# Performance work log

Hardware: AMD Instinct MI355X
Metric: run time of the kernel (lower is better)

## Reference

```python
import jax, jax.numpy as jnp
import numpy as np

R = 4            # num_runs
P_DROP = 0.2     # node dropout prob
BN_EPS = 1e-5
L = 2            # num_layers
D = 128          # hidden_channels
NA, NP_ = 50000, 100000
E = 500000


def setup_inputs() -> dict:
    key = jax.random.key(0)
    ks = jax.random.split(key, 20)
    s = 0.05
    x_author = jax.random.normal(ks[0], (NA, D), jnp.float32)
    x_paper = jax.random.normal(ks[1], (NP_, D), jnp.float32)
    # edge_index rows: [src, dst]
    ei_ap = jnp.stack([
        jax.random.randint(ks[2], (E,), 0, NA),
        jax.random.randint(ks[3], (E,), 0, NP_)]).astype(jnp.int64)
    ei_pa = jnp.stack([
        jax.random.randint(ks[4], (E,), 0, NP_),
        jax.random.randint(ks[5], (E,), 0, NA)]).astype(jnp.int64)
    # bernoulli(1-p) keep masks, one per run per node
    drop_author = (jax.random.uniform(ks[6], (R, NA)) < (1.0 - P_DROP)).astype(jnp.float32)
    drop_paper = (jax.random.uniform(ks[7], (R, NP_)) < (1.0 - P_DROP)).astype(jnp.float32)
    return {
        "x_author": x_author, "x_paper": x_paper,
        "ei_ap": ei_ap, "ei_pa": ei_pa,
        "drop_author": drop_author, "drop_paper": drop_paper,
        "lin_a_w": jax.random.normal(ks[8], (D, D)) * s,
        "lin_a_b": jnp.zeros((D,), jnp.float32),
        "lin_p_w": jax.random.normal(ks[9], (D, D)) * s,
        "lin_p_b": jnp.zeros((D,), jnp.float32),
        "W1": jax.random.normal(ks[10], (L, 2, D, D)) * s,
        "B1": jnp.zeros((L, 2, D), jnp.float32),
        "G": jnp.ones((L, 2, D), jnp.float32),
        "BT": jnp.zeros((L, 2, D), jnp.float32),
        "W2": jax.random.normal(ks[11], (L, 2, D, D)) * s,
        "B2": jnp.zeros((L, 2, D), jnp.float32),
        "EPS": jnp.zeros((L, 2), jnp.float32),  # GIN train_eps init 0
        "final_w": jax.random.normal(ks[12], (D, 4)) * s,
        "final_b": jnp.zeros((4,), jnp.float32),
    }


def _gin(x_src, x_dst, ei, eps, w1, b1, g, bt, w2, b2):
    # x_src: [Rs*Ns, D] flattened over runs; x_dst: [Rd*Nd, D]
    # scatter-sum neighbor messages into dst (only run-0 slots touched,
    # matching the original code which reuses the unexpanded edge_index)
    agg = jnp.zeros_like(x_dst).at[ei[1]].add(x_src[ei[0]])
    z = (1.0 + eps) * x_dst + agg
    h = z @ w1 + b1
    # BatchNorm1d, training-mode batch stats (biased variance)
    mu = h.mean(axis=0)
    var = ((h - mu) ** 2).mean(axis=0)
    h = (h - mu) * jax.lax.rsqrt(var + BN_EPS) * g + bt
    h = jax.nn.relu(h)
    return h @ w2 + b2


def reference(x_author, x_paper, ei_ap, ei_pa, drop_author, drop_paper,
              lin_a_w, lin_a_b, lin_p_w, lin_p_b,
              W1, B1, G, BT, W2, B2, EPS, final_w, final_b):
    inv_keep = 1.0 / (1.0 - P_DROP)
    # input projections, expand over runs, DropGNN node dropout
    h_a = x_author @ lin_a_w + lin_a_b                       # [Na, D]
    h_a = jnp.broadcast_to(h_a[None], (R,) + h_a.shape)      # [R, Na, D]
    h_a = h_a * drop_author[..., None] * inv_keep
    h_p = x_paper @ lin_p_w + lin_p_b
    h_p = jnp.broadcast_to(h_p[None], (R,) + h_p.shape)
    h_p = h_p * drop_paper[..., None] * inv_keep

    for l in range(L):
        xa = h_a.reshape(-1, D)
        xp = h_p.reshape(-1, D)
        # edge type 0: author -writes-> paper ; edge type 1: paper -> author
        new_p = _gin(xa, xp, ei_ap, EPS[l, 0], W1[l, 0], B1[l, 0], G[l, 0], BT[l, 0], W2[l, 0], B2[l, 0])
        new_a = _gin(xp, xa, ei_pa, EPS[l, 1], W1[l, 1], B1[l, 1], G[l, 1], BT[l, 1], W2[l, 1], B2[l, 1])
        h_a = jax.nn.relu(new_a.reshape(R, NA, D))
        h_p = jax.nn.relu(new_p.reshape(R, NP_, D))

    h = h_a.mean(axis=0)                                     # [Na, D]
    return h @ final_w + final_b                             # [Na, num_classes]
```

## Files before the change

kernel.cpp:

```cpp
#include <hip/hip_runtime.h>

#define NRUNS 4
#define NAU 50000
#define NPP 100000
#define NEDGE 500000
#define HD 128
#define INV_KEEP 1.25f
#define BN_EPS 1e-5f
#define LDA 136
#define NB_GEMM 1536

#define M_PROJ 0
#define M_GIN1 1
#define M_GIN2 2

typedef unsigned short bf16r;
typedef __attribute__((ext_vector_type(8))) short v8s;
typedef __attribute__((ext_vector_type(4))) float v4f;

__device__ inline float bf2f(bf16r u) {
    return __uint_as_float(((unsigned)u) << 16);
}
__device__ inline bf16r f2bf(float f) {
    __bf16 b = (__bf16)f;
    return __builtin_bit_cast(bf16r, b);
}

__global__ __launch_bounds__(256)
void zero_k(float* p, long n4) {
    long i = (long)blockIdx.x * 256 + threadIdx.x;
    long stride = (long)gridDim.x * 256;
    float4 z = make_float4(0.f, 0.f, 0.f, 0.f);
    for (; i < n4; i += stride) ((float4*)p)[i] = z;
}

__global__ __launch_bounds__(256)
void convw_k(const float* __restrict__ lin_a_w, const float* __restrict__ lin_p_w,
             const float* __restrict__ W1, const float* __restrict__ W2,
             bf16r* __restrict__ wt)
{
    int t = blockIdx.x >> 6;
    int e = (blockIdx.x & 63) * 256 + threadIdx.x;
    const float* src;
    if (t == 0) src = lin_a_w;
    else if (t == 1) src = lin_p_w;
    else if (t < 6) src = W1 + (size_t)(t - 2) * HD * HD;
    else src = W2 + (size_t)(t - 6) * HD * HD;
    int n = e >> 7, k = e & 127;
    wt[(size_t)t * HD * HD + e] = f2bf(src[(size_t)k * HD + n]);
}

__global__ __launch_bounds__(256)
void count_k(const int* __restrict__ ei, int E, int* cnt) {
    int e = blockIdx.x * 256 + threadIdx.x;
    if (e < E) atomicAdd(&cnt[ei[E + e]], 1);
}

__global__ __launch_bounds__(256)
void scan1_k(const int* __restrict__ in, int* out, int* partial, int n) {
    __shared__ int lds[256];
    int b = blockIdx.x, t = threadIdx.x;
    int base = b * 1024 + t * 4;
    int v0 = 0, v1 = 0, v2 = 0, v3 = 0;
    if (base + 3 < n) {
        int4 x = *(const int4*)(in + base);
        v0 = x.x; v1 = x.y; v2 = x.z; v3 = x.w;
    } else {
        if (base + 0 < n) v0 = in[base + 0];
        if (base + 1 < n) v1 = in[base + 1];
        if (base + 2 < n) v2 = in[base + 2];
        if (base + 3 < n) v3 = in[base + 3];
    }
    int s = v0 + v1 + v2 + v3;
    lds[t] = s;
    __syncthreads();
    for (int d = 1; d < 256; d <<= 1) {
        int x = (t >= d) ? lds[t - d] : 0;
        __syncthreads();
        lds[t] += x;
        __syncthreads();
    }
    int excl = lds[t] - s;
    if (base + 0 < n) out[base + 0] = excl;
    if (base + 1 < n) out[base + 1] = excl + v0;
    if (base + 2 < n) out[base + 2] = excl + v0 + v1;
    if (base + 3 < n) out[base + 3] = excl + v0 + v1 + v2;
    if (t == 255) partial[b] = lds[255];
}

__global__ __launch_bounds__(256)
void scan2_k(int* partial, int n) {
    __shared__ int lds[256];
    int t = threadIdx.x;
    int s = (t < n) ? partial[t] : 0;
    lds[t] = s;
    __syncthreads();
    for (int d = 1; d < 256; d <<= 1) {
        int x = (t >= d) ? lds[t - d] : 0;
        __syncthreads();
        lds[t] += x;
        __syncthreads();
    }
    if (t < n) partial[t] = lds[t] - s;
}

__global__ __launch_bounds__(256)
void scan3_k(int* off, int* cur, const int* __restrict__ partial, int n, int total) {
    int b = blockIdx.x, t = threadIdx.x;
    int add = partial[b];
    int base = b * 1024 + t * 4;
    #pragma unroll
    for (int j = 0; j < 4; ++j) {
        int i = base + j;
        if (i < n) {
            int v = off[i] + add;
            off[i] = v;
            cur[i] = v;
        }
    }
    if (b == 0 && t == 0) off[n] = total;
}

__global__ __launch_bounds__(256)
void fill_k(const int* __restrict__ ei, int E, int* cur, int* bucket) {
    int e = blockIdx.x * 256 + threadIdx.x;
    if (e < E) {
        int d = ei[E + e];
        int p = atomicAdd(&cur[d], 1);
        bucket[p] = ei[e];
    }
}

__global__ __launch_bounds__(256)
void gather2_k(const bf16r* __restrict__ hA, const bf16r* __restrict__ hP,
               bf16r* __restrict__ aggP, bf16r* __restrict__ aggA,
               const int* __restrict__ offAP, const int* __restrict__ bktAP,
               const int* __restrict__ offPA, const int* __restrict__ bktPA)
{
    int gw = (blockIdx.x * 256 + threadIdx.x) >> 6;
    int lane = threadIdx.x & 63;
    const bf16r* src; bf16r* agg; const int* off; const int* bkt; int w;
    if (gw < NPP) { src = hA; agg = aggP; off = offAP; bkt = bktAP; w = gw; }
    else          { src = hP; agg = aggA; off = offPA; bkt = bktPA; w = gw - NPP; }
    int s0 = off[w], s1 = off[w + 1];
    float a0 = 0.f, a1 = 0.f;
    int e = s0;
    for (; e + 1 < s1; e += 2) {
        int i0 = bkt[e], i1 = bkt[e + 1];
        ushort2 u = *(const ushort2*)(src + (size_t)i0 * HD + lane * 2);
        ushort2 v = *(const ushort2*)(src + (size_t)i1 * HD + lane * 2);
        a0 += bf2f(u.x) + bf2f(v.x);
        a1 += bf2f(u.y) + bf2f(v.y);
    }
    if (e < s1) {
        ushort2 u = *(const ushort2*)(src + (size_t)bkt[e] * HD + lane * 2);
        a0 += bf2f(u.x);
        a1 += bf2f(u.y);
    }
    ushort2 o;
    o.x = f2bf(a0);
    o.y = f2bf(a1);
    *(ushort2*)(agg + (size_t)w * HD + lane * 2) = o;
}

__global__ __launch_bounds__(256)
void scatter_k(const bf16r* __restrict__ src, float* dst,
               const int* __restrict__ ei, int E)
{
    int g = blockIdx.x * 256 + threadIdx.x;
    int e = g >> 5, lane = g & 31;
    if (e >= E) return;
    int s = ei[e], d = ei[E + e];
    ushort4 u = *(const ushort4*)(src + (size_t)s * HD + lane * 4);
    float* dp = dst + (size_t)d * HD + lane * 4;
    unsafeAtomicAdd(dp + 0, bf2f(u.x));
    unsafeAtomicAdd(dp + 1, bf2f(u.y));
    unsafeAtomicAdd(dp + 2, bf2f(u.z));
    unsafeAtomicAdd(dp + 3, bf2f(u.w));
}

struct SideP {
    const void* in;
    bf16r* out;
    const bf16r* wt;
    const float* bias;
    const void* agg;
    const float* epsp;
    float* gsum;
    float* gsumsq;
    const float* scale;
    const float* shift;
    const float* mask;
    int M, Nn, tiles;
};

template<int MODE, typename IT, typename AT>
__global__ __launch_bounds__(256)
void mfma_gemm(SideP P, SideP A, int BP)
{
    __shared__ bf16r za[64][LDA];
    __shared__ float red[2][HD];
    const int tid = threadIdx.x;

    SideP S;
    int t, tstride;
    if ((int)blockIdx.x < BP) { S = P; t = blockIdx.x; tstride = BP; }
    else { S = A; t = (int)blockIdx.x - BP; tstride = NB_GEMM - BP; }
    if (t >= S.tiles) return;

    const int wid = tid >> 6, lane = tid & 63;
    const int lr = lane & 15, lk = (lane >> 4) * 8;
    const int colq = (lane >> 4) * 4, cb = wid * 32;
    const int srow = tid >> 4;
    const int scol = (tid & 15) * 8;

    float epsv = 1.0f;
    if (MODE == M_GIN1) epsv = 1.0f + S.epsp[0];

    v8s w[2][4];
    #pragma unroll
    for (int cf = 0; cf < 2; ++cf)
        #pragma unroll
        for (int ks = 0; ks < 4; ++ks)
            w[cf][ks] = *(const v8s*)(S.wt + (size_t)(cb + cf * 16 + lr) * HD + ks * 32 + lk);

    const float4 bb0 = *(const float4*)(S.bias + cb + colq);
    const float4 bb1 = *(const float4*)(S.bias + cb + 16 + colq);

    float4 sc0h, sc1h, sh0h, sh1h;
    if (MODE == M_GIN2) {
        sc0h = *(const float4*)(S.scale + scol);
        sc1h = *(const float4*)(S.scale + scol + 4);
        sh0h = *(const float4*)(S.shift + scol);
        sh1h = *(const float4*)(S.shift + scol + 4);
    }

    float st_s[2][4], st_q[2][4];
    if (MODE == M_GIN1) {
        #pragma unroll
        for (int cf = 0; cf < 2; ++cf)
            #pragma unroll
            for (int j = 0; j < 4; ++j) { st_s[cf][j] = 0.f; st_q[cf][j] = 0.f; }
    }

    constexpr int NVH = (MODE == M_PROJ) ? 2 : 1;
    constexpr bool PAGG = (MODE == M_GIN1);
    constexpr int NVA = (PAGG && sizeof(AT) == 4) ? 2 : 1;
    int4 pre[4][NVH];
    int4 preA[4][NVA];

    auto prefetch = [&](int tt) {
        int m0n = tt * 64;
        #pragma unroll
        for (int i = 0; i < 4; ++i) {
            int gr = m0n + srow + 16 * i;
            if (gr < S.M) {
                const int4* p = (const int4*)((const IT*)S.in + (size_t)gr * HD + scol);
                pre[i][0] = p[0];
                if constexpr (NVH == 2) pre[i][1] = p[1];
            } else {
                pre[i][0] = make_int4(0, 0, 0, 0);
                if constexpr (NVH == 2) pre[i][1] = make_int4(0, 0, 0, 0);
            }
            if constexpr (PAGG) {
                if (gr < S.Nn) {
                    const int4* pa = (const int4*)((const AT*)S.agg + (size_t)gr * HD + scol);
                    preA[i][0] = pa[0];
                    if constexpr (NVA == 2) preA[i][1] = pa[1];
                } else {
                    preA[i][0] = make_int4(0, 0, 0, 0);
                    if constexpr (NVA == 2) preA[i][1] = make_int4(0, 0, 0, 0);
                }
            }
        }
    };

    prefetch(t);

    for (;;) {
        const int m0 = t * 64;
        #pragma unroll
        for (int i = 0; i < 4; ++i) {
            int row = srow + 16 * i;
            float v[8];
            if constexpr (NVH == 2) {
                const float* pf = (const float*)&pre[i][0];
                #pragma unroll
                for (int j = 0; j < 8; ++j) v[j] = pf[j];
            } else {
                const bf16r* pu = (const bf16r*)&pre[i][0];
                #pragma unroll
                for (int j = 0; j < 8; ++j) v[j] = bf2f(pu[j]);
            }
            if constexpr (MODE == M_GIN1) {
                float av[8];
                if constexpr (sizeof(AT) == 4) {
                    const float* pa = (const float*)&preA[i][0];
                    #pragma unroll
                    for (int j = 0; j < 8; ++j) av[j] = pa[j];
                } else {
                    const bf16r* pa = (const bf16r*)&preA[i][0];
                    #pragma unroll
                    for (int j = 0; j < 8; ++j) av[j] = bf2f(pa[j]);
                }
                #pragma unroll
                for (int j = 0; j < 8; ++j) v[j] = v[j] * epsv + av[j];
            } else if constexpr (MODE == M_GIN2) {
                v[0] = fmaxf(v[0] * sc0h.x + sh0h.x, 0.f);
                v[1] = fmaxf(v[1] * sc0h.y + sh0h.y, 0.f);
                v[2] = fmaxf(v[2] * sc0h.z + sh0h.z, 0.f);
                v[3] = fmaxf(v[3] * sc0h.w + sh0h.w, 0.f);
                v[4] = fmaxf(v[4] * sc1h.x + sh1h.x, 0.f);
                v[5] = fmaxf(v[5] * sc1h.y + sh1h.y, 0.f);
                v[6] = fmaxf(v[6] * sc1h.z + sh1h.z, 0.f);
                v[7] = fmaxf(v[7] * sc1h.w + sh1h.w, 0.f);
            }
            union { v8s w8; bf16r u[8]; } pk;
            #pragma unroll
            for (int j = 0; j < 8; ++j) pk.u[j] = f2bf(v[j]);
            *(v8s*)&za[row][scol] = pk.w8;
        }
        __syncthreads();

        const int tn = t + tstride;
        const bool more = tn < S.tiles;
        if (more) prefetch(tn);

        v4f acc[2][4];
        #pragma unroll
        for (int cf = 0; cf < 2; ++cf)
            #pragma unroll
            for (int rf = 0; rf < 4; ++rf) acc[cf][rf] = (v4f){0.f, 0.f, 0.f, 0.f};

        #pragma unroll
        for (int ks = 0; ks < 4; ++ks)
            #pragma unroll
            for (int rf = 0; rf < 4; ++rf) {
                v8s a = *(const v8s*)&za[rf * 16 + lr][ks * 32 + lk];
                acc[0][rf] = __builtin_amdgcn_mfma_f32_16x16x32_bf16(w[0][ks], a, acc[0][rf], 0, 0, 0);
                acc[1][rf] = __builtin_amdgcn_mfma_f32_16x16x32_bf16(w[1][ks], a, acc[1][rf], 0, 0, 0);
            }

        #pragma unroll
        for (int rf = 0; rf < 4; ++rf) {
            acc[0][rf][0] += bb0.x; acc[0][rf][1] += bb0.y;
            acc[0][rf][2] += bb0.z; acc[0][rf][3] += bb0.w;
            acc[1][rf][0] += bb1.x; acc[1][rf][1] += bb1.y;
            acc[1][rf][2] += bb1.z; acc[1][rf][3] += bb1.w;
        }

        if constexpr (MODE == M_PROJ) {
            #pragma unroll
            for (int rf = 0; rf < 4; ++rf) {
                int grow = m0 + rf * 16 + lr;
                if (grow < S.M) {
                    #pragma unroll
                    for (int run = 0; run < NRUNS; ++run) {
                        float wm = S.mask[(size_t)run * S.Nn + grow] * INV_KEEP;
                        #pragma unroll
                        for (int cf = 0; cf < 2; ++cf) {
                            ushort4 o;
                            o.x = f2bf(acc[cf][rf][0] * wm);
                            o.y = f2bf(acc[cf][rf][1] * wm);
                            o.z = f2bf(acc[cf][rf][2] * wm);
                            o.w = f2bf(acc[cf][rf][3] * wm);
                            *(ushort4*)(S.out + ((size_t)run * S.Nn + grow) * HD + cb + cf * 16 + colq) = o;
                        }
                    }
                }
            }
        } else if constexpr (MODE == M_GIN1) {
            #pragma unroll
            for (int rf = 0; rf < 4; ++rf) {
                int grow = m0 + rf * 16 + lr;
                #pragma unroll
                for (int cf = 0; cf < 2; ++cf) {
                    ushort4 o;
                    o.x = f2bf(acc[cf][rf][0]);
                    o.y = f2bf(acc[cf][rf][1]);
                    o.z = f2bf(acc[cf][rf][2]);
                    o.w = f2bf(acc[cf][rf][3]);
                    *(ushort4*)(S.out + (size_t)grow * HD + cb + cf * 16 + colq) = o;
                }
            }
            #pragma unroll
            for (int cf = 0; cf < 2; ++cf)
                #pragma unroll
                for (int j = 0; j < 4; ++j)
                    #pragma unroll
                    for (int rf = 0; rf < 4; ++rf) {
                        float vv = acc[cf][rf][j];
                        st_s[cf][j] += vv;
                        st_q[cf][j] += vv * vv;
                    }
        } else {
            #pragma unroll
            for (int rf = 0; rf < 4; ++rf) {
                int grow = m0 + rf * 16 + lr;
                #pragma unroll
                for (int cf = 0; cf < 2; ++cf) {
                    ushort4 o;
                    o.x = f2bf(fmaxf(acc[cf][rf][0], 0.f));
                    o.y = f2bf(fmaxf(acc[cf][rf][1], 0.f));
                    o.z = f2bf(fmaxf(acc[cf][rf][2], 0.f));
                    o.w = f2bf(fmaxf(acc[cf][rf][3], 0.f));
                    *(ushort4*)(S.out + (size_t)grow * HD + cb + cf * 16 + colq) = o;
                }
            }
        }

        if (!more) break;
        t = tn;
        __syncthreads();
    }

    if constexpr (MODE == M_GIN1) {
        #pragma unroll
        for (int d = 1; d < 16; d <<= 1)
            #pragma unroll
            for (int cf = 0; cf < 2; ++cf)
                #pragma unroll
                for (int j = 0; j < 4; ++j) {
                    st_s[cf][j] += __shfl_xor(st_s[cf][j], d);
                    st_q[cf][j] += __shfl_xor(st_q[cf][j], d);
                }
        if (lr == 0) {
            #pragma unroll
            for (int cf = 0; cf < 2; ++cf)
                #pragma unroll
                for (int j = 0; j < 4; ++j) {
                    red[0][cb + cf * 16 + colq + j] = st_s[cf][j];
                    red[1][cb + cf * 16 + colq + j] = st_q[cf][j];
                }
        }
        __syncthreads();
        if (tid < HD) {
            unsafeAtomicAdd(S.gsum + tid, red[0][tid]);
            unsafeAtomicAdd(S.gsumsq + tid, red[1][tid]);
        }
    }
}

__global__ void finalize2_k(float* gsP, float* gsqP, const float* gamP, const float* betP,
                            float* scP, float* shP, float invNP,
                            float* gsA, float* gsqA, const float* gamA, const float* betA,
                            float* scA, float* shA, float invNA)
{
    int c = threadIdx.x;
    float *gs, *gsq, *sc, *sh;
    const float *gm, *bt;
    float invN;
    if (c < HD) { gs = gsP; gsq = gsqP; gm = gamP; bt = betP; sc = scP; sh = shP; invN = invNP; }
    else { c -= HD; gs = gsA; gsq = gsqA; gm = gamA; bt = betA; sc = scA; sh = shA; invN = invNA; }
    float mu = gs[c] * invN;
    float var = gsq[c] * invN - mu * mu;
    float s = gm[c] * rsqrtf(var + BN_EPS);
    sc[c] = s;
    sh[c] = bt[c] - mu * s;
    gs[c] = 0.f;
    gsq[c] = 0.f;
}

__global__ __launch_bounds__(256)
void final_k(const bf16r* __restrict__ ha, const float* __restrict__ fw,
             const float* __restrict__ fb, float* __restrict__ out)
{
    int g = blockIdx.x * 256 + threadIdx.x;
    int node = g >> 6, lane = g & 63;
    if (node >= NAU) return;
    float m0 = 0.f, m1 = 0.f;
    #pragma unroll
    for (int r = 0; r < NRUNS; ++r) {
        size_t base = ((size_t)r * NAU + node) * HD;
        m0 += bf2f(ha[base + lane]);
        m1 += bf2f(ha[base + 64 + lane]);
    }
    m0 *= 0.25f;
    m1 *= 0.25f;
    float p[4];
    #pragma unroll
    for (int c = 0; c < 4; ++c)
        p[c] = m0 * fw[lane * 4 + c] + m1 * fw[(lane + 64) * 4 + c];
    #pragma unroll
    for (int off = 32; off >= 1; off >>= 1)
        #pragma unroll
        for (int c = 0; c < 4; ++c) p[c] += __shfl_down(p[c], off);
    if (lane == 0) {
        #pragma unroll
        for (int c = 0; c < 4; ++c) out[(size_t)node * 4 + c] = p[c] + fb[c];
    }
}

#define CSR_INTS ((size_t)(NPP + 4) + NEDGE + (NAU + 4) + NEDGE)
#define WT_ELEMS ((size_t)10 * HD * HD)

template<bool GATHER>
static void run_all(void* const* d_in, void* d_out, void* d_ws, hipStream_t stream)
{
    const float* x_author = (const float*)d_in[0];
    const float* x_paper  = (const float*)d_in[1];
    const int*   ei_ap    = (const int*)d_in[2];
    const int*   ei_pa    = (const int*)d_in[3];
    const float* drop_a   = (const float*)d_in[4];
    const float* drop_p   = (const float*)d_in[5];
    const float* lin_a_w  = (const float*)d_in[6];
    const float* lin_a_b  = (const float*)d_in[7];
    const float* lin_p_w  = (const float*)d_in[8];
    const float* lin_p_b  = (const float*)d_in[9];
    const float* W1       = (const float*)d_in[10];
    const float* B1       = (const float*)d_in[11];
    const float* G        = (const float*)d_in[12];
    const float* BT       = (const float*)d_in[13];
    const float* W2       = (const float*)d_in[14];
    const float* B2       = (const float*)d_in[15];
    const float* EPS      = (const float*)d_in[16];
    const float* fw       = (const float*)d_in[17];
    const float* fb       = (const float*)d_in[18];

    float* gsumP   = (float*)d_ws;
    float* gsumsqP = gsumP + HD;
    float* gsumA   = gsumP + 2 * HD;
    float* gsumsqA = gsumP + 3 * HD;
    float* scP     = gsumP + 4 * HD;
    float* shP     = gsumP + 5 * HD;
    float* scA     = gsumP + 6 * HD;
    float* shA     = gsumP + 7 * HD;
    bf16r* wt = (bf16r*)(gsumP + 8 * HD);
    char* cp = (char*)(wt + WT_ELEMS);

    int *off_ap = nullptr, *bkt_ap = nullptr, *off_pa = nullptr, *bkt_pa = nullptr;
    if (GATHER) {
        int* ip = (int*)cp;
        off_ap = ip;  ip += NPP + 4;
        bkt_ap = ip;  ip += NEDGE;
        off_pa = ip;  ip += NAU + 4;
        bkt_pa = ip;  ip += NEDGE;
        cp = (char*)ip;
    }
    void* agg_a_v = cp;
    size_t aggElem = GATHER ? sizeof(bf16r) : sizeof(float);
    void* agg_p_v = cp + (size_t)NAU * HD * aggElem;
    bf16r* h_a = (bf16r*)(cp + (size_t)(NAU + NPP) * HD * aggElem);
    bf16r* h_p = h_a + (size_t)NRUNS * NAU * HD;

    const bf16r* wt_lin_a = wt;
    const bf16r* wt_lin_p = wt + (size_t)1 * HD * HD;
    const bf16r* wt_W1    = wt + (size_t)2 * HD * HD;
    const bf16r* wt_W2    = wt + (size_t)6 * HD * HD;

    convw_k<<<640, 256, 0, stream>>>(lin_a_w, lin_p_w, W1, W2, wt);
    zero_k<<<1, 256, 0, stream>>>(gsumP, (4 * HD) / 4);

    if (GATHER) {
        int* cur_ap  = (int*)agg_a_v;
        int* cur_pa  = cur_ap + NPP;
        int* partial = cur_pa + NAU;
        {
            int nchunk = (NPP + 1023) / 1024;
            zero_k<<<64, 256, 0, stream>>>((float*)cur_ap, NPP / 4);
            count_k<<<(NEDGE + 255) / 256, 256, 0, stream>>>(ei_ap, NEDGE, cur_ap);
            scan1_k<<<nchunk, 256, 0, stream>>>(cur_ap, off_ap, partial, NPP);
            scan2_k<<<1, 256, 0, stream>>>(partial, nchunk);
            scan3_k<<<nchunk, 256, 0, stream>>>(off_ap, cur_ap, partial, NPP, NEDGE);
            fill_k<<<(NEDGE + 255) / 256, 256, 0, stream>>>(ei_ap, NEDGE, cur_ap, bkt_ap);
        }
        {
            int nchunk = (NAU + 1023) / 1024;
            zero_k<<<64, 256, 0, stream>>>((float*)cur_pa, NAU / 4);
            count_k<<<(NEDGE + 255) / 256, 256, 0, stream>>>(ei_pa, NEDGE, cur_pa);
            scan1_k<<<nchunk, 256, 0, stream>>>(cur_pa, off_pa, partial, NAU);
            scan2_k<<<1, 256, 0, stream>>>(partial, nchunk);
            scan3_k<<<nchunk, 256, 0, stream>>>(off_pa, cur_pa, partial, NAU, NEDGE);
            fill_k<<<(NEDGE + 255) / 256, 256, 0, stream>>>(ei_pa, NEDGE, cur_pa, bkt_pa);
        }
    }

    SideP Pp = {};
    Pp.in = x_paper; Pp.out = h_p; Pp.wt = wt_lin_p; Pp.bias = lin_p_b;
    Pp.mask = drop_p; Pp.M = NPP; Pp.Nn = NPP; Pp.tiles = (NPP + 63) / 64;
    SideP Pa = {};
    Pa.in = x_author; Pa.out = h_a; Pa.wt = wt_lin_a; Pa.bias = lin_a_b;
    Pa.mask = drop_a; Pa.M = NAU; Pa.Nn = NAU; Pa.tiles = (NAU + 63) / 64;
    int BPproj = (int)((long)NB_GEMM * Pp.tiles / (Pp.tiles + Pa.tiles));
    mfma_gemm<M_PROJ, float, bf16r><<<NB_GEMM, 256, 0, stream>>>(Pp, Pa, BPproj);

    const int TP = NRUNS * NPP / 64, TA = NRUNS * NAU / 64;
    const int BPgin = (int)((long)NB_GEMM * TP / (TP + TA));

    for (int l = 0; l < 2; ++l) {
        int t0 = l * 2 + 0, t1 = l * 2 + 1;

        if (GATHER) {
            gather2_k<<<((NPP + NAU) * 64) / 256, 256, 0, stream>>>(
                h_a, h_p, (bf16r*)agg_p_v, (bf16r*)agg_a_v,
                off_ap, bkt_ap, off_pa, bkt_pa);
        } else {
            zero_k<<<2048, 256, 0, stream>>>((float*)agg_a_v, ((size_t)(NAU + NPP) * HD) / 4);
            scatter_k<<<(NEDGE * 32) / 256, 256, 0, stream>>>(h_a, (float*)agg_p_v, ei_ap, NEDGE);
            scatter_k<<<(NEDGE * 32) / 256, 256, 0, stream>>>(h_p, (float*)agg_a_v, ei_pa, NEDGE);
        }

        SideP G1p = {};
        G1p.in = h_p; G1p.out = h_p; G1p.wt = wt_W1 + (size_t)t0 * HD * HD;
        G1p.bias = B1 + (size_t)t0 * HD; G1p.agg = agg_p_v; G1p.epsp = EPS + t0;
        G1p.gsum = gsumP; G1p.gsumsq = gsumsqP;
        G1p.M = NRUNS * NPP; G1p.Nn = NPP; G1p.tiles = TP;
        SideP G1a = {};
        G1a.in = h_a; G1a.out = h_a; G1a.wt = wt_W1 + (size_t)t1 * HD * HD;
        G1a.bias = B1 + (size_t)t1 * HD; G1a.agg = agg_a_v; G1a.epsp = EPS + t1;
        G1a.gsum = gsumA; G1a.gsumsq = gsumsqA;
        G1a.M = NRUNS * NAU; G1a.Nn = NAU; G1a.tiles = TA;
        if (GATHER)
            mfma_gemm<M_GIN1, bf16r, bf16r><<<NB_GEMM, 256, 0, stream>>>(G1p, G1a, BPgin);
        else
            mfma_gemm<M_GIN1, bf16r, float><<<NB_GEMM, 256, 0, stream>>>(G1p, G1a, BPgin);

        finalize2_k<<<1, 256, 0, stream>>>(
            gsumP, gsumsqP, G + (size_t)t0 * HD, BT + (size_t)t0 * HD, scP, shP,
            1.0f / (NRUNS * NPP),
            gsumA, gsumsqA, G + (size_t)t1 * HD, BT + (size_t)t1 * HD, scA, shA,
            1.0f / (NRUNS * NAU));

        SideP G2p = {};
        G2p.in = h_p; G2p.out = h_p; G2p.wt = wt_W2 + (size_t)t0 * HD * HD;
        G2p.bias = B2 + (size_t)t0 * HD; G2p.scale = scP; G2p.shift = shP;
        G2p.M = NRUNS * NPP; G2p.Nn = NPP; G2p.tiles = TP;
        SideP G2a = {};
        G2a.in = h_a; G2a.out = h_a; G2a.wt = wt_W2 + (size_t)t1 * HD * HD;
        G2a.bias = B2 + (size_t)t1 * HD; G2a.scale = scA; G2a.shift = shA;
        G2a.M = NRUNS * NAU; G2a.Nn = NAU; G2a.tiles = TA;
        mfma_gemm<M_GIN2, bf16r, bf16r><<<NB_GEMM, 256, 0, stream>>>(G2p, G2a, BPgin);
    }

    final_k<<<(NAU * 64) / 256, 256, 0, stream>>>(h_a, fw, fb, (float*)d_out);
}

extern "C" void kernel_launch(void* const* d_in, const int* in_sizes, int n_in,
                              void* d_out, int out_size, void* d_ws, size_t ws_size,
                              hipStream_t stream)
{
    const size_t hB    = (size_t)NRUNS * (NAU + NPP) * HD * sizeof(bf16r);
    const size_t statB = 8 * HD * sizeof(float);
    const size_t wtB   = WT_ELEMS * sizeof(bf16r);
    const size_t csrB  = CSR_INTS * sizeof(int);
    const size_t aggBF = (size_t)(NAU + NPP) * HD * sizeof(bf16r);

    const size_t need_gather = statB + wtB + csrB + aggBF + hB;
    if (ws_size >= need_gather) {
        run_all<true>(d_in, d_out, d_ws, stream);
    } else {
        run_all<false>(d_in, d_out, d_ws, stream);
    }
}
```

Measured before the change: 650.0 us.

## Fuse CSR gather and dropout into GIN1 GEMM, merge CSR-build and finalize kernels

The projection GEMM now writes a single unexpanded bf16 copy. The first GIN GEMM applies dropout masks on the fly and gathers neighbour rows through the CSR directly, so the separate gather kernel and the aggregate buffer are gone. BatchNorm scale and shift are computed inside the second GEMM, replacing the finalize kernel. The CSR-build, weight-conversion and zeroing kernels are merged across both edge types, and the GEMM grid size is lowered. The cost is more irregular gathers inside the GEMM's load phase, which may stall the MFMA pipeline and unbalance work across blocks.

```diff
diff --git a/kernel.cpp b/kernel.cpp
--- a/kernel.cpp
+++ b/kernel.cpp
@@ -8,11 +8,17 @@
 #define INV_KEEP 1.25f
 #define BN_EPS 1e-5f
 #define LDA 136
-#define NB_GEMM 1536
-
-#define M_PROJ 0
-#define M_GIN1 1
-#define M_GIN2 2
+#define NB_GEMM 1280
+
+#define M_PROJ   0
+#define M_GIN1   1
+#define M_GIN2   2
+#define M_PROJ1  3
+#define M_GIN1F0 4
+#define M_GIN1F1 5
+
+#define C_AP ((NPP + 1023) / 1024)
+#define C_PA ((NAU + 1023) / 1024)
 
 typedef unsigned short bf16r;
 typedef __attribute__((ext_vector_type(8))) short v8s;
@@ -35,32 +41,49 @@
 }
 
 __global__ __launch_bounds__(256)
-void convw_k(const float* __restrict__ lin_a_w, const float* __restrict__ lin_p_w,
-             const float* __restrict__ W1, const float* __restrict__ W2,
-             bf16r* __restrict__ wt)
-{
-    int t = blockIdx.x >> 6;
-    int e = (blockIdx.x & 63) * 256 + threadIdx.x;
-    const float* src;
-    if (t == 0) src = lin_a_w;
-    else if (t == 1) src = lin_p_w;
-    else if (t < 6) src = W1 + (size_t)(t - 2) * HD * HD;
-    else src = W2 + (size_t)(t - 6) * HD * HD;
-    int n = e >> 7, k = e & 127;
-    wt[(size_t)t * HD * HD + e] = f2bf(src[(size_t)k * HD + n]);
-}
-
-__global__ __launch_bounds__(256)
-void count_k(const int* __restrict__ ei, int E, int* cnt) {
-    int e = blockIdx.x * 256 + threadIdx.x;
-    if (e < E) atomicAdd(&cnt[ei[E + e]], 1);
-}
-
-__global__ __launch_bounds__(256)
-void scan1_k(const int* __restrict__ in, int* out, int* partial, int n) {
+void convw_prep_k(const float* __restrict__ lin_a_w, const float* __restrict__ lin_p_w,
+                  const float* __restrict__ W1, const float* __restrict__ W2,
+                  bf16r* __restrict__ wt, float* __restrict__ stats,
+                  float* __restrict__ curz, int curz4)
+{
+    int b = blockIdx.x;
+    if (b < 640) {
+        int t = b >> 6;
+        int e = (b & 63) * 256 + threadIdx.x;
+        const float* src;
+        if (t == 0) src = lin_a_w;
+        else if (t == 1) src = lin_p_w;
+        else if (t < 6) src = W1 + (size_t)(t - 2) * HD * HD;
+        else src = W2 + (size_t)(t - 6) * HD * HD;
+        int n = e >> 7, k = e & 127;
+        wt[(size_t)t * HD * HD + e] = f2bf(src[(size_t)k * HD + n]);
+    } else if (b == 640) {
+        ((float4*)stats)[threadIdx.x] = make_float4(0.f, 0.f, 0.f, 0.f);
+    } else {
+        int i = (b - 641) * 256 + threadIdx.x;
+        if (i < curz4) ((float4*)curz)[i] = make_float4(0.f, 0.f, 0.f, 0.f);
+    }
+}
+
+__global__ __launch_bounds__(256)
+void count2_k(const int* __restrict__ ei_ap, const int* __restrict__ ei_pa,
+              int* curA, int* curB)
+{
+    int g = blockIdx.x * 256 + threadIdx.x;
+    if (g < NEDGE) atomicAdd(&curA[ei_ap[NEDGE + g]], 1);
+    else if (g < 2 * NEDGE) atomicAdd(&curB[ei_pa[NEDGE + (g - NEDGE)]], 1);
+}
+
+__global__ __launch_bounds__(256)
+void scan1m_k(const int* __restrict__ curA, int* offA,
+              const int* __restrict__ curB, int* offB, int* partial)
+{
     __shared__ int lds[256];
     int b = blockIdx.x, t = threadIdx.x;
-    int base = b * 1024 + t * 4;
+    const int* in; int* out; int n, chunk;
+    if (b < C_AP) { in = curA; out = offA; n = NPP; chunk = b; }
+    else          { in = curB; out = offB; n = NAU; chunk = b - C_AP; }
+    int base = chunk * 1024 + t * 4;
     int v0 = 0, v1 = 0, v2 = 0, v3 = 0;
     if (base + 3 < n) {
         int4 x = *(const int4*)(in + base);
@@ -89,10 +112,13 @@
 }
 
 __global__ __launch_bounds__(256)
-void scan2_k(int* partial, int n) {
+void scan2m_k(int* partial)
+{
     __shared__ int lds[256];
     int t = threadIdx.x;
-    int s = (t < n) ? partial[t] : 0;
+    int base = blockIdx.x == 0 ? 0 : C_AP;
+    int n = blockIdx.x == 0 ? C_AP : C_PA;
+    int s = (t < n) ? partial[base + t] : 0;
     lds[t] = s;
     __syncthreads();
     for (int d = 1; d < 256; d <<= 1) {
@@ -101,14 +127,19 @@
         lds[t] += x;
         __syncthreads();
     }
-    if (t < n) partial[t] = lds[t] - s;
-}
-
-__global__ __launch_bounds__(256)
-void scan3_k(int* off, int* cur, const int* __restrict__ partial, int n, int total) {
+    if (t < n) partial[base + t] = lds[t] - s;
+}
+
+__global__ __launch_bounds__(256)
+void scan3m_k(int* offA, int* curA, int* offB, int* curB,
+              const int* __restrict__ partial)
+{
     int b = blockIdx.x, t = threadIdx.x;
+    int* off; int* cur; int n, chunk;
+    if (b < C_AP) { off = offA; cur = curA; n = NPP; chunk = b; }
+    else          { off = offB; cur = curB; n = NAU; chunk = b - C_AP; }
     int add = partial[b];
-    int base = b * 1024 + t * 4;
+    int base = chunk * 1024 + t * 4;
     #pragma unroll
     for (int j = 0; j < 4; ++j) {
         int i = base + j;
@@ -118,49 +149,22 @@
             cur[i] = v;
         }
     }
-    if (b == 0 && t == 0) off[n] = total;
-}
-
-__global__ __launch_bounds__(256)
-void fill_k(const int* __restrict__ ei, int E, int* cur, int* bucket) {
-    int e = blockIdx.x * 256 + threadIdx.x;
-    if (e < E) {
-        int d = ei[E + e];
-        int p = atomicAdd(&cur[d], 1);
-        bucket[p] = ei[e];
-    }
-}
-
-__global__ __launch_bounds__(256)
-void gather2_k(const bf16r* __restrict__ hA, const bf16r* __restrict__ hP,
-               bf16r* __restrict__ aggP, bf16r* __restrict__ aggA,
-               const int* __restrict__ offAP, const int* __restrict__ bktAP,
-               const int* __restrict__ offPA, const int* __restrict__ bktPA)
-{
-    int gw = (blockIdx.x * 256 + threadIdx.x) >> 6;
-    int lane = threadIdx.x & 63;
-    const bf16r* src; bf16r* agg; const int* off; const int* bkt; int w;
-    if (gw < NPP) { src = hA; agg = aggP; off = offAP; bkt = bktAP; w = gw; }
-    else          { src = hP; agg = aggA; off = offPA; bkt = bktPA; w = gw - NPP; }
-    int s0 = off[w], s1 = off[w + 1];
-    float a0 = 0.f, a1 = 0.f;
-    int e = s0;
-    for (; e + 1 < s1; e += 2) {
-        int i0 = bkt[e], i1 = bkt[e + 1];
-        ushort2 u = *(const ushort2*)(src + (size_t)i0 * HD + lane * 2);
-        ushort2 v = *(const ushort2*)(src + (size_t)i1 * HD + lane * 2);
-        a0 += bf2f(u.x) + bf2f(v.x);
-        a1 += bf2f(u.y) + bf2f(v.y);
-    }
-    if (e < s1) {
-        ushort2 u = *(const ushort2*)(src + (size_t)bkt[e] * HD + lane * 2);
-        a0 += bf2f(u.x);
-        a1 += bf2f(u.y);
-    }
-    ushort2 o;
-    o.x = f2bf(a0);
-    o.y = f2bf(a1);
-    *(ushort2*)(agg + (size_t)w * HD + lane * 2) = o;
+    if (chunk == 0 && t == 0) off[n] = NEDGE;
+}
+
+__global__ __launch_bounds__(256)
+void fill2_k(const int* __restrict__ ei_ap, const int* __restrict__ ei_pa,
+             int* curA, int* bktA, int* curB, int* bktB)
+{
+    int g = blockIdx.x * 256 + threadIdx.x;
+    if (g < NEDGE) {
+        int d = ei_ap[NEDGE + g];
+        bktA[atomicAdd(&curA[d], 1)] = ei_ap[g];
+    } else if (g < 2 * NEDGE) {
+        int e = g - NEDGE;
+        int d = ei_pa[NEDGE + e];
+        bktB[atomicAdd(&curB[d], 1)] = ei_pa[e];
+    }
 }
 
 __global__ __launch_bounds__(256)
@@ -181,15 +185,22 @@
 
 struct SideP {
     const void* in;
+    const void* in2;
     bf16r* out;
+    bf16r* out2;
+    const bf16r* src;
+    const int* off;
+    const int* bkt;
+    const float* msk0;
     const bf16r* wt;
     const float* bias;
     const void* agg;
     const float* epsp;
     float* gsum;
     float* gsumsq;
-    const float* scale;
-    const float* shift;
+    const float* gamma;
+    const float* beta;
+    float invN;
     const float* mask;
     int M, Nn, tiles;
 };
@@ -208,6 +219,12 @@
     else { S = A; t = (int)blockIdx.x - BP; tstride = NB_GEMM - BP; }
     if (t >= S.tiles) return;
 
+    constexpr bool FUSED   = (MODE == M_GIN1F0 || MODE == M_GIN1F1);
+    constexpr bool MASKF   = (MODE == M_GIN1F0);
+    constexpr bool GIN1ANY = (MODE == M_GIN1 || FUSED);
+    constexpr int  NVH     = (MODE == M_PROJ || MODE == M_PROJ1) ? 2 : 1;
+    constexpr bool PAGG    = (MODE == M_GIN1);
+
     const int wid = tid >> 6, lane = tid & 63;
     const int lr = lane & 15, lk = (lane >> 4) * 8;
     const int colq = (lane >> 4) * 4, cb = wid * 32;
@@ -215,7 +232,7 @@
     const int scol = (tid & 15) * 8;
 
     float epsv = 1.0f;
-    if (MODE == M_GIN1) epsv = 1.0f + S.epsp[0];
+    if (GIN1ANY) epsv = 1.0f + S.epsp[0];
 
     v8s w[2][4];
     #pragma unroll
@@ -227,34 +244,53 @@
     const float4 bb0 = *(const float4*)(S.bias + cb + colq);
     const float4 bb1 = *(const float4*)(S.bias + cb + 16 + colq);
 
-    float4 sc0h, sc1h, sh0h, sh1h;
-    if (MODE == M_GIN2) {
-        sc0h = *(const float4*)(S.scale + scol);
-        sc1h = *(const float4*)(S.scale + scol + 4);
-        sh0h = *(const float4*)(S.shift + scol);
-        sh1h = *(const float4*)(S.shift + scol + 4);
+    float sc8[MODE == M_GIN2 ? 8 : 1], sh8[MODE == M_GIN2 ? 8 : 1];
+    if constexpr (MODE == M_GIN2) {
+        #pragma unroll
+        for (int j = 0; j < 8; ++j) {
+            int c = scol + j;
+            float mu = S.gsum[c] * S.invN;
+            float var = S.gsumsq[c] * S.invN - mu * mu;
+            float s = S.gamma[c] * rsqrtf(var + BN_EPS);
+            sc8[j] = s;
+            sh8[j] = S.beta[c] - mu * s;
+        }
     }
 
     float st_s[2][4], st_q[2][4];
-    if (MODE == M_GIN1) {
+    if (GIN1ANY) {
         #pragma unroll
         for (int cf = 0; cf < 2; ++cf)
             #pragma unroll
             for (int j = 0; j < 4; ++j) { st_s[cf][j] = 0.f; st_q[cf][j] = 0.f; }
     }
 
-    constexpr int NVH = (MODE == M_PROJ) ? 2 : 1;
-    constexpr bool PAGG = (MODE == M_GIN1);
     constexpr int NVA = (PAGG && sizeof(AT) == 4) ? 2 : 1;
     int4 pre[4][NVH];
     int4 preA[4][NVA];
+    float mpre[MASKF ? 4 : 1];
+    int2 offv[FUSED ? 4 : 1];
 
     auto prefetch = [&](int tt) {
         int m0n = tt * 64;
         #pragma unroll
         for (int i = 0; i < 4; ++i) {
             int gr = m0n + srow + 16 * i;
-            if (gr < S.M) {
+            if constexpr (FUSED) {
+                int run = (gr >= S.Nn) + (gr >= 2 * S.Nn) + (gr >= 3 * S.Nn);
+                size_t sidx = MASKF ? (size_t)(gr - run * S.Nn) : (size_t)gr;
+                pre[i][0] = *(const int4*)((const bf16r*)S.in + sidx * HD + scol);
+                if constexpr (MASKF) mpre[i] = S.mask[gr];
+                if (gr < S.Nn) {
+                    offv[i].x = S.off[gr];
+                    offv[i].y = S.off[gr + 1];
+                } else {
+                    offv[i] = make_int2(0, 0);
+                }
+            } else if constexpr (MODE == M_GIN2) {
+                const IT* base = (const IT*)((gr < S.Nn) ? S.in2 : S.in);
+                pre[i][0] = *(const int4*)(base + (size_t)gr * HD + scol);
+            } else if (gr < S.M) {
                 const int4* p = (const int4*)((const IT*)S.in + (size_t)gr * HD + scol);
                 pre[i][0] = p[0];
                 if constexpr (NVH == 2) pre[i][1] = p[1];
@@ -292,7 +328,28 @@
                 #pragma unroll
                 for (int j = 0; j < 8; ++j) v[j] = bf2f(pu[j]);
             }
-            if constexpr (MODE == M_GIN1) {
+            if constexpr (FUSED) {
+                float coef = epsv;
+                if constexpr (MASKF) coef *= mpre[i] * INV_KEEP;
+                float g[8];
+                #pragma unroll
+                for (int j = 0; j < 8; ++j) g[j] = 0.f;
+                int s0 = offv[i].x, s1 = offv[i].y;
+                for (int e = s0; e < s1; ++e) {
+                    int idx = S.bkt[e];
+                    float m = 1.0f;
+                    if constexpr (MASKF) m = S.msk0[idx] * INV_KEEP;
+                    const bf16r* rp = S.src + (size_t)idx * HD + scol;
+                    ushort4 u0 = *(const ushort4*)rp;
+                    ushort4 u1 = *(const ushort4*)(rp + 4);
+                    g[0] += m * bf2f(u0.x); g[1] += m * bf2f(u0.y);
+                    g[2] += m * bf2f(u0.z); g[3] += m * bf2f(u0.w);
+                    g[4] += m * bf2f(u1.x); g[5] += m * bf2f(u1.y);
+                    g[6] += m * bf2f(u1.z); g[7] += m * bf2f(u1.w);
+                }
+                #pragma unroll
+                for (int j = 0; j < 8; ++j) v[j] = v[j] * coef + g[j];
+            } else if constexpr (MODE == M_GIN1) {
                 float av[8];
                 if constexpr (sizeof(AT) == 4) {
                     const float* pa = (const float*)&preA[i][0];
@@ -306,14 +363,9 @@
                 #pragma unroll
                 for (int j = 0; j < 8; ++j) v[j] = v[j] * epsv + av[j];
             } else if constexpr (MODE == M_GIN2) {
-                v[0] = fmaxf(v[0] * sc0h.x + sh0h.x, 0.f);
-                v[1] = fmaxf(v[1] * sc0h.y + sh0h.y, 0.f);
-                v[2] = fmaxf(v[2] * sc0h.z + sh0h.z, 0.f);
-                v[3] = fmaxf(v[3] * sc0h.w + sh0h.w, 0.f);
-                v[4] = fmaxf(v[4] * sc1h.x + sh1h.x, 0.f);
-                v[5] = fmaxf(v[5] * sc1h.y + sh1h.y, 0.f);
-                v[6] = fmaxf(v[6] * sc1h.z + sh1h.z, 0.f);
-                v[7] = fmaxf(v[7] * sc1h.w + sh1h.w, 0.f);
+                #pragma unroll
+                for (int j = 0; j < 8; ++j)
+                    v[j] = fmaxf(v[j] * sc8[j] + sh8[j], 0.f);
             }
             union { v8s w8; bf16r u[8]; } pk;
             #pragma unroll
@@ -369,10 +421,30 @@
                     }
                 }
             }
-        } else if constexpr (MODE == M_GIN1) {
+        } else if constexpr (MODE == M_PROJ1) {
             #pragma unroll
             for (int rf = 0; rf < 4; ++rf) {
                 int grow = m0 + rf * 16 + lr;
+                if (grow < S.M) {
+                    #pragma unroll
+                    for (int cf = 0; cf < 2; ++cf) {
+                        ushort4 o;
+                        o.x = f2bf(acc[cf][rf][0]);
+                        o.y = f2bf(acc[cf][rf][1]);
+                        o.z = f2bf(acc[cf][rf][2]);
+                        o.w = f2bf(acc[cf][rf][3]);
+                        *(ushort4*)(S.out + (size_t)grow * HD + cb + cf * 16 + colq) = o;
+                    }
+                }
+            }
+        } else if constexpr (GIN1ANY) {
+            #pragma unroll
+            for (int rf = 0; rf < 4; ++rf) {
+                int grow = m0 + rf * 16 + lr;
+                bf16r* ob = S.out;
+                if constexpr (MODE == M_GIN1F1) {
+                    if (grow < S.Nn) ob = S.out2;
+                }
                 #pragma unroll
                 for (int cf = 0; cf < 2; ++cf) {
                     ushort4 o;
@@ -380,7 +452,7 @@
                     o.y = f2bf(acc[cf][rf][1]);
                     o.z = f2bf(acc[cf][rf][2]);
                     o.w = f2bf(acc[cf][rf][3]);
-                    *(ushort4*)(S.out + (size_t)grow * HD + cb + cf * 16 + colq) = o;
+                    *(ushort4*)(ob + (size_t)grow * HD + cb + cf * 16 + colq) = o;
                 }
             }
             #pragma unroll
@@ -414,7 +486,7 @@
         __syncthreads();
     }
 
-    if constexpr (MODE == M_GIN1) {
+    if constexpr (GIN1ANY) {
         #pragma unroll
         for (int d = 1; d < 16; d <<= 1)
             #pragma unroll
@@ -439,26 +511,6 @@
             unsafeAtomicAdd(S.gsumsq + tid, red[1][tid]);
         }
     }
-}
-
-__global__ void finalize2_k(float* gsP, float* gsqP, const float* gamP, const float* betP,
-                            float* scP, float* shP, float invNP,
-                            float* gsA, float* gsqA, const float* gamA, const float* betA,
-                            float* scA, float* shA, float invNA)
-{
-    int c = threadIdx.x;
-    float *gs, *gsq, *sc, *sh;
-    const float *gm, *bt;
-    float invN;
-    if (c < HD) { gs = gsP; gsq = gsqP; gm = gamP; bt = betP; sc = scP; sh = shP; invN = invNP; }
-    else { c -= HD; gs = gsA; gsq = gsqA; gm = gamA; bt = betA; sc = scA; sh = shA; invN = invNA; }
-    float mu = gs[c] * invN;
-    float var = gsq[c] * invN - mu * mu;
-    float s = gm[c] * rsqrtf(var + BN_EPS);
-    sc[c] = s;
-    sh[c] = bt[c] - mu * s;
-    gs[c] = 0.f;
-    gsq[c] = 0.f;
 }
 
 __global__ __launch_bounds__(256)
@@ -517,15 +569,8 @@
     const float* fw       = (const float*)d_in[17];
     const float* fb       = (const float*)d_in[18];
 
-    float* gsumP   = (float*)d_ws;
-    float* gsumsqP = gsumP + HD;
-    float* gsumA   = gsumP + 2 * HD;
-    float* gsumsqA = gsumP + 3 * HD;
-    float* scP     = gsumP + 4 * HD;
-    float* shP     = gsumP + 5 * HD;
-    float* scA     = gsumP + 6 * HD;
-    float* shA     = gsumP + 7 * HD;
-    bf16r* wt = (bf16r*)(gsumP + 8 * HD);
+    float* stats = (float*)d_ws;
+    bf16r* wt = (bf16r*)(stats + 8 * HD);
     char* cp = (char*)(wt + WT_ELEMS);
 
     int *off_ap = nullptr, *bkt_ap = nullptr, *off_pa = nullptr, *bkt_pa = nullptr;
@@ -537,10 +582,18 @@
         bkt_pa = ip;  ip += NEDGE;
         cp = (char*)ip;
     }
-    void* agg_a_v = cp;
-    size_t aggElem = GATHER ? sizeof(bf16r) : sizeof(float);
-    void* agg_p_v = cp + (size_t)NAU * HD * aggElem;
-    bf16r* h_a = (bf16r*)(cp + (size_t)(NAU + NPP) * HD * aggElem);
+
+    bf16r* alt_a = nullptr; bf16r* alt_p = nullptr;
+    void* agg_a_v = nullptr; void* agg_p_v = nullptr;
+    if (GATHER) {
+        alt_a = (bf16r*)cp;  cp += (size_t)NAU * HD * sizeof(bf16r);
+        alt_p = (bf16r*)cp;  cp += (size_t)NPP * HD * sizeof(bf16r);
+    } else {
+        agg_a_v = cp;
+        agg_p_v = cp + (size_t)NAU * HD * sizeof(float);
+        cp += (size_t)(NAU + NPP) * HD * sizeof(float);
+    }
+    bf16r* h_a = (bf16r*)cp;
     bf16r* h_p = h_a + (size_t)NRUNS * NAU * HD;
 
     const bf16r* wt_lin_a = wt;
@@ -548,88 +601,116 @@
     const bf16r* wt_W1    = wt + (size_t)2 * HD * HD;
     const bf16r* wt_W2    = wt + (size_t)6 * HD * HD;
 
-    convw_k<<<640, 256, 0, stream>>>(lin_a_w, lin_p_w, W1, W2, wt);
-    zero_k<<<1, 256, 0, stream>>>(gsumP, (4 * HD) / 4);
+    int* cur_ap = GATHER ? (int*)alt_a : (int*)agg_a_v;
+    int* cur_pa = cur_ap + NPP;
+    int* partial = cur_pa + NAU;
+
+    convw_prep_k<<<788, 256, 0, stream>>>(lin_a_w, lin_p_w, W1, W2, wt, stats,
+                                          (float*)cur_ap, (NPP + NAU) / 4);
 
     if (GATHER) {
-        int* cur_ap  = (int*)agg_a_v;
-        int* cur_pa  = cur_ap + NPP;
-        int* partial = cur_pa + NAU;
-        {
-            int nchunk = (NPP + 1023) / 1024;
-            zero_k<<<64, 256, 0, stream>>>((float*)cur_ap, NPP / 4);
-            count_k<<<(NEDGE + 255) / 256, 256, 0, stream>>>(ei_ap, NEDGE, cur_ap);
-            scan1_k<<<nchunk, 256, 0, stream>>>(cur_ap, off_ap, partial, NPP);
-            scan2_k<<<1, 256, 0, stream>>>(partial, nchunk);
-            scan3_k<<<nchunk, 256, 0, stream>>>(off_ap, cur_ap, partial, NPP, NEDGE);
-            fill_k<<<(NEDGE + 255) / 256, 256, 0, stream>>>(ei_ap, NEDGE, cur_ap, bkt_ap);
-        }
-        {
-            int nchunk = (NAU + 1023) / 1024;
-            zero_k<<<64, 256, 0, stream>>>((float*)cur_pa, NAU / 4);
-            count_k<<<(NEDGE + 255) / 256, 256, 0, stream>>>(ei_pa, NEDGE, cur_pa);
-            scan1_k<<<nchunk, 256, 0, stream>>>(cur_pa, off_pa, partial, NAU);
-            scan2_k<<<1, 256, 0, stream>>>(partial, nchunk);
-            scan3_k<<<nchunk, 256, 0, stream>>>(off_pa, cur_pa, partial, NAU, NEDGE);
-            fill_k<<<(NEDGE + 255) / 256, 256, 0, stream>>>(ei_pa, NEDGE, cur_pa, bkt_pa);
-        }
-    }
-
-    SideP Pp = {};
-    Pp.in = x_paper; Pp.out = h_p; Pp.wt = wt_lin_p; Pp.bias = lin_p_b;
-    Pp.mask = drop_p; Pp.M = NPP; Pp.Nn = NPP; Pp.tiles = (NPP + 63) / 64;
-    SideP Pa = {};
-    Pa.in = x_author; Pa.out = h_a; Pa.wt = wt_lin_a; Pa.bias = lin_a_b;
-    Pa.mask = drop_a; Pa.M = NAU; Pa.Nn = NAU; Pa.tiles = (NAU + 63) / 64;
-    int BPproj = (int)((long)NB_GEMM * Pp.tiles / (Pp.tiles + Pa.tiles));
-    mfma_gemm<M_PROJ, float, bf16r><<<NB_GEMM, 256, 0, stream>>>(Pp, Pa, BPproj);
+        count2_k<<<(2 * NEDGE + 255) / 256, 256, 0, stream>>>(ei_ap, ei_pa, cur_ap, cur_pa);
+        scan1m_k<<<C_AP + C_PA, 256, 0, stream>>>(cur_ap, off_ap, cur_pa, off_pa, partial);
+        scan2m_k<<<2, 256, 0, stream>>>(partial);
+        scan3m_k<<<C_AP + C_PA, 256, 0, stream>>>(off_ap, cur_ap, off_pa, cur_pa, partial);
+        fill2_k<<<(2 * NEDGE + 255) / 256, 256, 0, stream>>>(ei_ap, ei_pa,
+                                                             cur_ap, bkt_ap, cur_pa, bkt_pa);
+    }
 
     const int TP = NRUNS * NPP / 64, TA = NRUNS * NAU / 64;
     const int BPgin = (int)((long)NB_GEMM * TP / (TP + TA));
 
-    for (int l = 0; l < 2; ++l) {
-        int t0 = l * 2 + 0, t1 = l * 2 + 1;
-
-        if (GATHER) {
-            gather2_k<<<((NPP + NAU) * 64) / 256, 256, 0, stream>>>(
-                h_a, h_p, (bf16r*)agg_p_v, (bf16r*)agg_a_v,
-                off_ap, bkt_ap, off_pa, bkt_pa);
-        } else {
+    if (GATHER) {
+        SideP Pp = {}, Pa = {};
+        Pp.in = x_paper; Pp.out = alt_p; Pp.wt = wt_lin_p; Pp.bias = lin_p_b;
+        Pp.M = NPP; Pp.Nn = NPP; Pp.tiles = (NPP + 63) / 64;
+        Pa.in = x_author; Pa.out = alt_a; Pa.wt = wt_lin_a; Pa.bias = lin_a_b;
+        Pa.M = NAU; Pa.Nn = NAU; Pa.tiles = (NAU + 63) / 64;
+        int BPproj = (int)((long)NB_GEMM * Pp.tiles / (Pp.tiles + Pa.tiles));
+        mfma_gemm<M_PROJ1, float, float><<<NB_GEMM, 256, 0, stream>>>(Pp, Pa, BPproj);
+
+        for (int l = 0; l < 2; ++l) {
+            int t0 = l * 2 + 0, t1 = l * 2 + 1;
+
+            SideP G1p = {}, G1a = {};
+            G1p.wt = wt_W1 + (size_t)t0 * HD * HD;
+            G1p.bias = B1 + (size_t)t0 * HD; G1p.epsp = EPS + t0;
+            G1p.gsum = stats + t0 * 2 * HD; G1p.gsumsq = G1p.gsum + HD;
+            G1p.M = NRUNS * NPP; G1p.Nn = NPP; G1p.tiles = TP;
+            G1p.out = h_p; G1p.off = off_ap; G1p.bkt = bkt_ap;
+            G1a.wt = wt_W1 + (size_t)t1 * HD * HD;
+            G1a.bias = B1 + (size_t)t1 * HD; G1a.epsp = EPS + t1;
+            G1a.gsum = stats + t1 * 2 * HD; G1a.gsumsq = G1a.gsum + HD;
+            G1a.M = NRUNS * NAU; G1a.Nn = NAU; G1a.tiles = TA;
+            G1a.out = h_a; G1a.off = off_pa; G1a.bkt = bkt_pa;
+            if (l == 0) {
+                G1p.in = alt_p; G1p.mask = drop_p; G1p.src = alt_a; G1p.msk0 = drop_a;
+                G1a.in = alt_a; G1a.mask = drop_a; G1a.src = alt_p; G1a.msk0 = drop_p;
+                mfma_gemm<M_GIN1F0, bf16r, float><<<NB_GEMM, 256, 0, stream>>>(G1p, G1a, BPgin);
+            } else {
+                G1p.in = h_p; G1p.src = h_a; G1p.out2 = alt_p;
+                G1a.in = h_a; G1a.src = h_p; G1a.out2 = alt_a;
+                mfma_gemm<M_GIN1F1, bf16r, float><<<NB_GEMM, 256, 0, stream>>>(G1p, G1a, BPgin);
+            }
+
+            SideP G2p = {}, G2a = {};
+            G2p.in = h_p; G2p.in2 = (l == 0) ? (const void*)h_p : (const void*)alt_p;
+            G2p.out = h_p; G2p.wt = wt_W2 + (size_t)t0 * HD * HD;
+            G2p.bias = B2 + (size_t)t0 * HD;
+            G2p.gsum = stats + t0 * 2 * HD; G2p.gsumsq = G2p.gsum + HD;
+            G2p.gamma = G + (size_t)t0 * HD; G2p.beta = BT + (size_t)t0 * HD;
+            G2p.invN = 1.0f / (NRUNS * NPP);
+            G2p.M = NRUNS * NPP; G2p.Nn = NPP; G2p.tiles = TP;
+            G2a.in = h_a; G2a.in2 = (l == 0) ? (const void*)h_a : (const void*)alt_a;
+            G2a.out = h_a; G2a.wt = wt_W2 + (size_t)t1 * HD * HD;
+            G2a.bias = B2 + (size_t)t1 * HD;
+            G2a.gsum = stats + t1 * 2 * HD; G2a.gsumsq = G2a.gsum + HD;
+            G2a.gamma = G + (size_t)t1 * HD; G2a.beta = BT + (size_t)t1 * HD;
+            G2a.invN = 1.0f / (NRUNS * NAU);
+            G2a.M = NRUNS * NAU; G2a.Nn = NAU; G2a.tiles = TA;
+            mfma_gemm<M_GIN2, bf16r, float><<<NB_GEMM, 256, 0, stream>>>(G2p, G2a, BPgin);
+        }
+    } else {
+        SideP Pp = {}, Pa = {};
+        Pp.in = x_paper; Pp.out = h_p; Pp.wt = wt_lin_p; Pp.bias = lin_p_b;
+        Pp.mask = drop_p; Pp.M = NPP; Pp.Nn = NPP; Pp.tiles = (NPP + 63) / 64;
+        Pa.in = x_author; Pa.out = h_a; Pa.wt = wt_lin_a; Pa.bias = lin_a_b;
+        Pa.mask = drop_a; Pa.M = NAU; Pa.Nn = NAU; Pa.tiles = (NAU + 63) / 64;
+        int BPproj = (int)((long)NB_GEMM * Pp.tiles / (Pp.tiles + Pa.tiles));
+        mfma_gemm<M_PROJ, float, float><<<NB_GEMM, 256, 0, stream>>>(Pp, Pa, BPproj);
+
+        for (int l = 0; l < 2; ++l) {
+            int t0 = l * 2 + 0, t1 = l * 2 + 1;
             zero_k<<<2048, 256, 0, stream>>>((float*)agg_a_v, ((size_t)(NAU + NPP) * HD) / 4);
             scatter_k<<<(NEDGE * 32) / 256, 256, 0, stream>>>(h_a, (float*)agg_p_v, ei_ap, NEDGE);
             scatter_k<<<(NEDGE * 32) / 256, 256, 0, stream>>>(h_p, (float*)agg_a_v, ei_pa, NEDGE);
-        }
-
-        SideP G1p = {};
-        G1p.in = h_p; G1p.out = h_p; G1p.wt = wt_W1 + (size_t)t0 * HD * HD;
-        G1p.bias = B1 + (size_t)t0 * HD; G1p.agg = agg_p_v; G1p.epsp = EPS + t0;
-        G1p.gsum = gsumP; G1p.gsumsq = gsumsqP;
-        G1p.M = NRUNS * NPP; G1p.Nn = NPP; G1p.tiles = TP;
-        SideP G1a = {};
-        G1a.in = h_a; G1a.out = h_a; G1a.wt = wt_W1 + (size_t)t1 * HD * HD;
-        G1a.bias = B1 + (size_t)t1 * HD; G1a.agg = agg_a_v; G1a.epsp = EPS + t1;
-        G1a.gsum = gsumA; G1a.gsumsq = gsumsqA;
-        G1a.M = NRUNS * NAU; G1a.Nn = NAU; G1a.tiles = TA;
-        if (GATHER)
-            mfma_gemm<M_GIN1, bf16r, bf16r><<<NB_GEMM, 256, 0, stream>>>(G1p, G1a, BPgin);
-        else
+
+            SideP G1p = {}, G1a = {};
+            G1p.in = h_p; G1p.out = h_p; G1p.wt = wt_W1 + (size_t)t0 * HD * HD;
+            G1p.bias = B1 + (size_t)t0 * HD; G1p.agg = agg_p_v; G1p.epsp = EPS + t0;
+            G1p.gsum = stats + t0 * 2 * HD; G1p.gsumsq = G1p.gsum + HD;
+            G1p.M = NRUNS * NPP; G1p.Nn = NPP; G1p.tiles = TP;
+            G1a.in = h_a; G1a.out = h_a; G1a.wt = wt_W1 + (size_t)t1 * HD * HD;
+            G1a.bias = B1 + (size_t)t1 * HD; G1a.agg = agg_a_v; G1a.epsp = EPS + t1;
+            G1a.gsum = stats + t1 * 2 * HD; G1a.gsumsq = G1a.gsum + HD;
+            G1a.M = NRUNS * NAU; G1a.Nn = NAU; G1a.tiles = TA;
             mfma_gemm<M_GIN1, bf16r, float><<<NB_GEMM, 256, 0, stream>>>(G1p, G1a, BPgin);
 
-        finalize2_k<<<1, 256, 0, stream>>>(
-            gsumP, gsumsqP, G + (size_t)t0 * HD, BT + (size_t)t0 * HD, scP, shP,
-            1.0f / (NRUNS * NPP),
-            gsumA, gsumsqA, G + (size_t)t1 * HD, BT + (size_t)t1 * HD, scA, shA,
-            1.0f / (NRUNS * NAU));
-
-        SideP G2p = {};
-        G2p.in = h_p; G2p.out = h_p; G2p.wt = wt_W2 + (size_t)t0 * HD * HD;
-        G2p.bias = B2 + (size_t)t0 * HD; G2p.scale = scP; G2p.shift = shP;
-        G2p.M = NRUNS * NPP; G2p.Nn = NPP; G2p.tiles = TP;
-        SideP G2a = {};
-        G2a.in = h_a; G2a.out = h_a; G2a.wt = wt_W2 + (size_t)t1 * HD * HD;
-        G2a.bias = B2 + (size_t)t1 * HD; G2a.scale = scA; G2a.shift = shA;
-        G2a.M = NRUNS * NAU; G2a.Nn = NAU; G2a.tiles = TA;
-        mfma_gemm<M_GIN2, bf16r, bf16r><<<NB_GEMM, 256, 0, stream>>>(G2p, G2a, BPgin);
+            SideP G2p = {}, G2a = {};
+            G2p.in = h_p; G2p.in2 = h_p; G2p.out = h_p;
+            G2p.wt = wt_W2 + (size_t)t0 * HD * HD; G2p.bias = B2 + (size_t)t0 * HD;
+            G2p.gsum = stats + t0 * 2 * HD; G2p.gsumsq = G2p.gsum + HD;
+            G2p.gamma = G + (size_t)t0 * HD; G2p.beta = BT + (size_t)t0 * HD;
+            G2p.invN = 1.0f / (NRUNS * NPP);
+            G2p.M = NRUNS * NPP; G2p.Nn = NPP; G2p.tiles = TP;
+            G2a.in = h_a; G2a.in2 = h_a; G2a.out = h_a;
+            G2a.wt = wt_W2 + (size_t)t1 * HD * HD; G2a.bias = B2 + (size_t)t1 * HD;
+            G2a.gsum = stats + t1 * 2 * HD; G2a.gsumsq = G2a.gsum + HD;
+            G2a.gamma = G + (size_t)t1 * HD; G2a.beta = BT + (size_t)t1 * HD;
+            G2a.invN = 1.0f / (NRUNS * NAU);
+            G2a.M = NRUNS * NAU; G2a.Nn = NAU; G2a.tiles = TA;
+            mfma_gemm<M_GIN2, bf16r, float><<<NB_GEMM, 256, 0, stream>>>(G2p, G2a, BPgin);
+        }
     }
 
     final_k<<<(NAU * 64) / 256, 256, 0, stream>>>(h_a, fw, fb, (float*)d_out);
@@ -643,9 +724,9 @@
     const size_t statB = 8 * HD * sizeof(float);
     const size_t wtB   = WT_ELEMS * sizeof(bf16r);
     const size_t csrB  = CSR_INTS * sizeof(int);
-    const size_t aggBF = (size_t)(NAU + NPP) * HD * sizeof(bf16r);
-
-    const size_t need_gather = statB + wtB + csrB + aggBF + hB;
+    const size_t altB  = (size_t)(NAU + NPP) * HD * sizeof(bf16r);
+
+    const size_t need_gather = statB + wtB + csrB + altB + hB;
     if (ws_size >= need_gather) {
         run_all<true>(d_in, d_out, d_ws, stream);
     } else {
```

Result: slower. 752.2 us (+15.7%).
